# Performance work log

Hardware: AMD Instinct MI355X
Metric: run time of the kernel (lower is better)

Reference implementation:

```python
import jax, jax.numpy as jnp
import numpy as np

N = 4096   # in_features
M = 4096   # out_features
RANK, FT_RANK = 128, 64
Q_SCALE, R_SCALE, L_SCALE, GLOBAL_SCALE = 0.9, 1.05, 1.1, 1.0


def fwht(x):
    """Normalized fast Walsh-Hadamard transform over last dim (power of 2).
    Matches matmul_hadU/hadUt for power-of-2 sizes (H symmetric, 1/sqrt(n))."""
    B, n = x.shape
    y, h = x, 1
    while h < n:
        y = y.reshape(B, n // (2 * h), 2, h)
        a, b = y[:, :, 0, :], y[:, :, 1, :]
        y = jnp.stack((a + b, a - b), axis=2)
        h *= 2
    return y.reshape(B, n) * (1.0 / np.sqrt(n)).astype(np.float32)


def dequant(grid, idxs, scale, n_cols):
    # E8P dequant: gather 8-dim lattice vectors, reshape to [rows, n_cols].
    return grid[idxs].reshape(idxs.shape[0], n_cols) * jnp.float32(scale)


def setup_inputs() -> dict:
    key = jax.random.key(0)
    ks = jax.random.split(key, 9)
    return {
        "x": jax.random.normal(ks[0], (4, 2048, N), jnp.float32),
        "SU": jnp.sign(jax.random.normal(ks[1], (N,), jnp.float32)),
        "SV": jnp.sign(jax.random.normal(ks[2], (M,), jnp.float32)),
        "grid": jax.random.normal(ks[3], (65536, 8), jnp.float32) * 0.05,
        "L_ft": jax.random.normal(ks[4], (M, FT_RANK), jnp.float32) * 0.05,
        "R_ft": jax.random.normal(ks[5], (FT_RANK, N), jnp.float32) * 0.05,
        "Q_idxs": jax.random.randint(ks[6], (M, N // 8), 0, 65536, jnp.int32),
        "R_idxs": jax.random.randint(ks[7], (RANK - FT_RANK, N // 8), 0, 65536, jnp.int32),
        "L_idxs": jax.random.randint(ks[8], (RANK - FT_RANK, M // 8), 0, 65536, jnp.int32),
    }


def reference(x, SU, SV, grid, L_ft, R_ft, Q_idxs, R_idxs, L_idxs):
    shape = x.shape
    xf = x.reshape(-1, N) * SU            # [T, n]
    xh = fwht(xf)                          # left randomized Hadamard (hadUt)
    # Q path (x/32 then *scale*32 cancels; applied via scale on W).
    W_q = dequant(grid, Q_idxs, Q_SCALE, N)          # [m, n]
    out = xh @ W_q.T                                  # [T, m]
    # Quantized low-rank path: xR = x @ W_R^T; out += xR @ W_L (transposed L).
    W_r = dequant(grid, R_idxs, R_SCALE, N)           # [r, n]
    W_l = dequant(grid, L_idxs, L_SCALE, M)           # [r, m]
    xR = xh @ W_r.T                                   # [T, r]
    out = out + xR @ W_l                              # [T, m]
    # Fine-tunable LoRA path.
    out = out + (xh @ R_ft.T) @ L_ft.T                # [T, m]
    out = fwht(out)                                   # right Hadamard (hadU)
    out = out * SV * jnp.float32(GLOBAL_SCALE)
    return out.reshape(shape[:-1] + (M,))
```

## Files before the change

kernel.cpp:

```cpp
#include <hip/hip_runtime.h>
#include <stdint.h>
#include <stddef.h>


typedef __attribute__((ext_vector_type(8))) __bf16 bf16x8;
typedef __attribute__((ext_vector_type(4))) float f32x4;

#define DEVFN static __device__ __forceinline__

typedef const __attribute__((address_space(1))) void* as1cvp;
typedef __attribute__((address_space(3))) void* as3vp;

DEVFN void async_g2l16(const void* g, void* l) {
  __builtin_amdgcn_global_load_lds((as1cvp)g, (as3vp)l, 16, 0, 0);
}

DEVFN void fwht16(float* v) {
  #pragma unroll
  for (int h = 1; h < 16; h <<= 1) {
    #pragma unroll
    for (int i = 0; i < 16; ++i) {
      if ((i & h) == 0) {
        float a = v[i], b = v[i + h];
        v[i] = a + b;
        v[i + h] = a - b;
      }
    }
  }
}

DEVFN int padi(int i) { return i + (i >> 4) + (i >> 8); }

template<int MODE>
__global__ __launch_bounds__(256)
void fwht_rows(const float* in, const float* __restrict__ sgn,
               __bf16* __restrict__ outb, float* outf)
{
  __shared__ float s[4366];
  const int row = blockIdx.x;
  const int t = threadIdx.x;
  const int base1 = t * 17 + (t >> 4);
  float v[16];

  {
    const float* src = in + (size_t)row * 4096 + t * 16;
    #pragma unroll
    for (int j4 = 0; j4 < 4; ++j4) {
      f32x4 xv = *(const f32x4*)(src + j4 * 4);
      #pragma unroll
      for (int q = 0; q < 4; ++q) v[j4 * 4 + q] = xv[q];
    }
  }
  if (MODE == 0) {
    const f32x4* sg4 = (const f32x4*)(sgn + t * 16);
    #pragma unroll
    for (int j4 = 0; j4 < 4; ++j4) {
      f32x4 sv = sg4[j4];
      #pragma unroll
      for (int q = 0; q < 4; ++q) v[j4 * 4 + q] *= sv[q];
    }
  }
  fwht16(v);
  #pragma unroll
  for (int j = 0; j < 16; ++j) s[base1 + j] = v[j];
  __syncthreads();

  const int base2 = (t & 15) + ((t >> 4) << 8);
  #pragma unroll
  for (int i = 0; i < 16; ++i) v[i] = s[padi(base2 + (i << 4))];
  fwht16(v);
  #pragma unroll
  for (int i = 0; i < 16; ++i) s[padi(base2 + (i << 4))] = v[i];
  __syncthreads();

  #pragma unroll
  for (int i = 0; i < 16; ++i) v[i] = s[padi(t + (i << 8))];
  fwht16(v);
  #pragma unroll
  for (int i = 0; i < 16; ++i) s[padi(t + (i << 8))] = v[i];
  __syncthreads();

  if (MODE == 0) {
    bf16x8 o0, o1;
    #pragma unroll
    for (int j = 0; j < 8; ++j) o0[j] = (__bf16)(s[base1 + j] * 0.015625f);
    #pragma unroll
    for (int j = 0; j < 8; ++j) o1[j] = (__bf16)(s[base1 + 8 + j] * 0.015625f);
    __bf16* dst = outb + (size_t)row * 4096 + t * 16;
    *(bf16x8*)dst = o0;
    *(bf16x8*)(dst + 8) = o1;
  } else {
    const f32x4* sg4 = (const f32x4*)(sgn + t * 16);
    float* dst = outf + (size_t)row * 4096 + t * 16;
    #pragma unroll
    for (int j4 = 0; j4 < 4; ++j4) {
      f32x4 sv = sg4[j4];
      f32x4 ov;
      #pragma unroll
      for (int q = 0; q < 4; ++q) ov[q] = s[base1 + j4 * 4 + q] * 0.015625f * sv[q];
      *(f32x4*)(dst + j4 * 4) = ov;
    }
  }
}

__global__ __launch_bounds__(256)
void prep_uv(const float* __restrict__ grid8,
             const float* __restrict__ Lft, const float* __restrict__ Rft,
             const int* __restrict__ Lidx, const int* __restrict__ Ridx,
             __bf16* __restrict__ Ut, __bf16* __restrict__ Vt)
{
  int tid = blockIdx.x * 256 + threadIdx.x;
  const int half = 4096 * 128;
  bool isV = tid >= half;
  int e = isV ? tid - half : tid;
  int j = e >> 7;
  int r = e & 127;
  float v;
  if (!isV) {
    if (r < 64) v = 1.1f * grid8[(size_t)Lidx[r * 512 + (j >> 3)] * 8 + (j & 7)];
    else        v = Lft[(size_t)j * 64 + (r - 64)];
    Ut[e] = (__bf16)v;
  } else {
    if (r < 64) v = 1.05f * grid8[(size_t)Ridx[r * 512 + (j >> 3)] * 8 + (j & 7)];
    else        v = Rft[(size_t)(r - 64) * 4096 + j];
    Vt[e] = (__bf16)v;
  }
}

template<int K>
__global__ __launch_bounds__(256)
void gemm_bt(const __bf16* __restrict__ A, const __bf16* __restrict__ B,
             __bf16* __restrict__ Cb,
             const int* __restrict__ Qidx, const float* __restrict__ grid8,
             int Nn, int nbx)
{
  __shared__ __bf16 sA[128 * 64];
  __shared__ __bf16 sB[128 * 64];

  const int nwg = gridDim.x;
  const int orig = blockIdx.x;
  const int cpx = nwg >> 3;
  const int wg = (orig & 7) * cpx + (orig >> 3);
  const int bm = wg / nbx, bn = wg % nbx;

  const int t = threadIdx.x;
  const int lane = t & 63;
  const int w = t >> 6;
  const int wr = w >> 1, wc = w & 1;

  const int aRow0 = bm * 128;
  const int bRow0 = bn * 128;

  f32x4 acc[4][4] = {};

  #pragma unroll 1
  for (int k0 = 0; k0 < K; k0 += 64) {
    #pragma unroll
    for (int i = 0; i < 4; ++i) {
      int u = i * 256 + t;
      int rowu = u >> 3, cs = u & 7;
      int c = cs ^ (rowu & 7);
      async_g2l16(A + (size_t)(aRow0 + rowu) * K + k0 + c * 8, &sA[u * 8]);
      async_g2l16(B + (size_t)(bRow0 + rowu) * K + k0 + c * 8, &sB[u * 8]);
    }
    asm volatile("s_waitcnt vmcnt(0)" ::: "memory");
    __syncthreads();

    bf16x8 a[4][2], b[4][2];
    #pragma unroll
    for (int m = 0; m < 4; ++m) {
      #pragma unroll
      for (int kk = 0; kk < 2; ++kk) {
        int c = kk * 4 + (lane >> 4);
        int rowA = wr * 64 + m * 16 + (lane & 15);
        int uA = rowA * 8 + (c ^ (rowA & 7));
        a[m][kk] = *(const bf16x8*)&sA[uA * 8];
        int rowB = wc * 64 + m * 16 + (lane & 15);
        int uB = rowB * 8 + (c ^ (rowB & 7));
        b[m][kk] = *(const bf16x8*)&sB[uB * 8];
      }
    }
    #pragma unroll
    for (int kk = 0; kk < 2; ++kk)
      #pragma unroll
      for (int m = 0; m < 4; ++m)
        #pragma unroll
        for (int n = 0; n < 4; ++n)
          acc[m][n] = __builtin_amdgcn_mfma_f32_16x16x32_bf16(
              a[m][kk], b[n][kk], acc[m][n], 0, 0, 0);
    __syncthreads();
  }

  #pragma unroll
  for (int m = 0; m < 4; ++m) {
    #pragma unroll
    for (int n = 0; n < 4; ++n) {
      int gr = aRow0 + wr * 64 + m * 16 + ((lane >> 4) << 2);
      int gc = bRow0 + wc * 64 + n * 16 + (lane & 15);
      #pragma unroll
      for (int q = 0; q < 4; ++q) {
        float v = acc[m][n][q];
        int idx = Qidx[(size_t)(gr + q) * (Nn >> 3) + (gc >> 3)];
        v += 0.9f * grid8[(size_t)idx * 8 + (gc & 7)];
        Cb[(size_t)(gr + q) * Nn + gc] = (__bf16)v;
      }
    }
  }
}

template<int NT>
__global__ __launch_bounds__(512, 2)
void gemm256(const __bf16* __restrict__ A, const __bf16* __restrict__ B,
             float* __restrict__ Cf, int Nn, int nbx)
{
  constexpr int K = NT * 32;
  __shared__ __bf16 lds[4 * 2 * 8192];

  const int nwg = gridDim.x;
  const int orig = blockIdx.x;
  const int cpx = nwg >> 3;
  const int wg = (orig & 7) * cpx + (orig >> 3);
  const int bm = wg / nbx, bn = wg % nbx;

  const int tid = threadIdx.x;
  const int lane = tid & 63;
  const int wid = tid >> 6;
  const int wm = wid >> 2;
  const int wn = wid & 3;

  const int aRow0 = bm * 256;
  const int bRow0 = bn * 256;

  auto stage = [&](int t) {
    __bf16* dA = &lds[((t & 3) * 2 + 0) * 8192];
    __bf16* dB = &lds[((t & 3) * 2 + 1) * 8192];
    const __bf16* sAg = A + (size_t)aRow0 * K + t * 32;
    const __bf16* sBg = B + (size_t)bRow0 * K + t * 32;
    #pragma unroll
    for (int i = 0; i < 2; ++i) {
      int u = i * 512 + tid;
      int prow = u >> 3, slot = u & 7;
      int chunk = slot ^ (prow & 7);
      int r = 2 * prow + (chunk >> 2);
      int k8 = chunk & 3;
      async_g2l16(sAg + (size_t)r * K + k8 * 8, dA + u * 8);
    }
    #pragma unroll
    for (int i = 0; i < 2; ++i) {
      int u = i * 512 + tid;
      int prow = u >> 3, slot = u & 7;
      int chunk = slot ^ (prow & 7);
      int r = 2 * prow + (chunk >> 2);
      int k8 = chunk & 3;
      async_g2l16(sBg + (size_t)r * K + k8 * 8, dB + u * 8);
    }
  };

  const int k8l = lane >> 4;
  const int rl = lane & 15;

  f32x4 acc[8][4] = {};

  stage(0); stage(1); stage(2);
  asm volatile("s_waitcnt vmcnt(8)" ::: "memory");
  __syncthreads();

  #pragma unroll 1
  for (int t = 0; t < NT; ++t) {
    if (t + 3 < NT) stage(t + 3);

    const __bf16* bufA = &lds[((t & 3) * 2 + 0) * 8192];
    const __bf16* bufB = &lds[((t & 3) * 2 + 1) * 8192];

    bf16x8 af[8], bfr[4];
    #pragma unroll
    for (int m = 0; m < 8; ++m) {
      int r = wm * 128 + m * 16 + rl;
      int prow = r >> 1;
      int slot = (((r & 1) << 2) | k8l) ^ (prow & 7);
      af[m] = *(const bf16x8*)(bufA + (prow * 8 + slot) * 8);
    }
    #pragma unroll
    for (int n = 0; n < 4; ++n) {
      int r = wn * 64 + n * 16 + rl;
      int prow = r >> 1;
      int slot = (((r & 1) << 2) | k8l) ^ (prow & 7);
      bfr[n] = *(const bf16x8*)(bufB + (prow * 8 + slot) * 8);
    }

    __builtin_amdgcn_s_setprio(1);
    #pragma unroll
    for (int m = 0; m < 8; ++m)
      #pragma unroll
      for (int n = 0; n < 4; ++n)
        acc[m][n] = __builtin_amdgcn_mfma_f32_16x16x32_bf16(
            af[m], bfr[n], acc[m][n], 0, 0, 0);
    __builtin_amdgcn_s_setprio(0);

    if (t + 3 < NT)      asm volatile("s_waitcnt vmcnt(8)" ::: "memory");
    else if (t + 2 < NT) asm volatile("s_waitcnt vmcnt(4)" ::: "memory");
    else if (t + 1 < NT) asm volatile("s_waitcnt vmcnt(0)" ::: "memory");
    __syncthreads();
  }

  #pragma unroll
  for (int m = 0; m < 8; ++m) {
    #pragma unroll
    for (int n = 0; n < 4; ++n) {
      int gr = aRow0 + wm * 128 + m * 16 + ((lane >> 4) << 2);
      int gc = bRow0 + wn * 64 + n * 16 + (lane & 15);
      #pragma unroll
      for (int q = 0; q < 4; ++q)
        Cf[(size_t)(gr + q) * Nn + gc] = acc[m][n][q];
    }
  }
}

extern "C" void kernel_launch(void* const* d_in, const int* in_sizes, int n_in,
                              void* d_out, int out_size, void* d_ws, size_t ws_size,
                              hipStream_t stream) {
  const float* x    = (const float*)d_in[0];
  const float* SU   = (const float*)d_in[1];
  const float* SV   = (const float*)d_in[2];
  const float* grid = (const float*)d_in[3];
  const float* Lft  = (const float*)d_in[4];
  const float* Rft  = (const float*)d_in[5];
  const int*   Qidx = (const int*)d_in[6];
  const int*   Ridx = (const int*)d_in[7];
  const int*   Lidx = (const int*)d_in[8];
  float* out = (float*)d_out;

  char* ws = (char*)d_ws;
  __bf16* xh = (__bf16*)ws;
  __bf16* Wc = (__bf16*)(ws + ((size_t)64 << 20));
  __bf16* Ut = (__bf16*)(ws + ((size_t)96 << 20));
  __bf16* Vt = (__bf16*)(ws + ((size_t)97 << 20));

  prep_uv<<<4096, 256, 0, stream>>>(grid, Lft, Rft, Lidx, Ridx, Ut, Vt);
  fwht_rows<0><<<8192, 256, 0, stream>>>(x, SU, xh, nullptr);
  gemm_bt<128><<<1024, 256, 0, stream>>>(Ut, Vt, Wc, Qidx, grid, 4096, 32);
  gemm256<128><<<512, 512, 0, stream>>>(xh, Wc, out, 4096, 16);
  fwht_rows<1><<<8192, 256, 0, stream>>>(out, SV, nullptr, out);
}
```

Measured before the change: 589.6 us.

## Restructure main GEMM into 8-phase ping-pong pipeline and batch FWHT rows per block

The main bf16 GEMM now uses K-tiles of 64 with double buffering instead of K=32 with a 4-stage ring. Each iteration is split into four MFMA quadrants, with LDS fragment loads and the next tile's global-to-LDS copies interleaved between explicit barriers, to overlap memory traffic with matrix-core work. The FWHT row kernel now handles 4 rows per block, loading signs once and prefetching the next row while the current one finishes. It also writes the last butterfly stage directly from registers with strided stores, dropping one LDS round trip. Risks are extra barriers, register pressure from the larger fragment arrays, and less coalesced output stores in the FWHT kernel.

```diff
diff --git a/kernel.cpp b/kernel.cpp
--- a/kernel.cpp
+++ b/kernel.cpp
@@ -34,72 +34,82 @@
 template<int MODE>
 __global__ __launch_bounds__(256)
 void fwht_rows(const float* in, const float* __restrict__ sgn,
-               __bf16* __restrict__ outb, float* outf)
+               __bf16* __restrict__ outb, float* __restrict__ outf)
 {
   __shared__ float s[4366];
-  const int row = blockIdx.x;
   const int t = threadIdx.x;
   const int base1 = t * 17 + (t >> 4);
-  float v[16];
-
+  const int base2 = (t & 15) + ((t >> 4) << 8);
+
+  float sg[16];
+  if (MODE == 0) {
+    const f32x4* p = (const f32x4*)(sgn + t * 16);
+    #pragma unroll
+    for (int j4 = 0; j4 < 4; ++j4) {
+      f32x4 sv = p[j4];
+      #pragma unroll
+      for (int q = 0; q < 4; ++q) sg[j4 * 4 + q] = sv[q];
+    }
+  } else {
+    #pragma unroll
+    for (int i = 0; i < 16; ++i) sg[i] = sgn[t + (i << 8)];
+  }
+
+  float v[16], w[16];
+  const int row0 = blockIdx.x * 4;
   {
-    const float* src = in + (size_t)row * 4096 + t * 16;
+    const f32x4* p = (const f32x4*)(in + (size_t)row0 * 4096 + t * 16);
     #pragma unroll
     for (int j4 = 0; j4 < 4; ++j4) {
-      f32x4 xv = *(const f32x4*)(src + j4 * 4);
+      f32x4 xv = p[j4];
       #pragma unroll
       for (int q = 0; q < 4; ++q) v[j4 * 4 + q] = xv[q];
     }
   }
-  if (MODE == 0) {
-    const f32x4* sg4 = (const f32x4*)(sgn + t * 16);
-    #pragma unroll
-    for (int j4 = 0; j4 < 4; ++j4) {
-      f32x4 sv = sg4[j4];
-      #pragma unroll
-      for (int q = 0; q < 4; ++q) v[j4 * 4 + q] *= sv[q];
-    }
-  }
-  fwht16(v);
-  #pragma unroll
-  for (int j = 0; j < 16; ++j) s[base1 + j] = v[j];
-  __syncthreads();
-
-  const int base2 = (t & 15) + ((t >> 4) << 8);
-  #pragma unroll
-  for (int i = 0; i < 16; ++i) v[i] = s[padi(base2 + (i << 4))];
-  fwht16(v);
-  #pragma unroll
-  for (int i = 0; i < 16; ++i) s[padi(base2 + (i << 4))] = v[i];
-  __syncthreads();
-
-  #pragma unroll
-  for (int i = 0; i < 16; ++i) v[i] = s[padi(t + (i << 8))];
-  fwht16(v);
-  #pragma unroll
-  for (int i = 0; i < 16; ++i) s[padi(t + (i << 8))] = v[i];
-  __syncthreads();
-
-  if (MODE == 0) {
-    bf16x8 o0, o1;
-    #pragma unroll
-    for (int j = 0; j < 8; ++j) o0[j] = (__bf16)(s[base1 + j] * 0.015625f);
-    #pragma unroll
-    for (int j = 0; j < 8; ++j) o1[j] = (__bf16)(s[base1 + 8 + j] * 0.015625f);
-    __bf16* dst = outb + (size_t)row * 4096 + t * 16;
-    *(bf16x8*)dst = o0;
-    *(bf16x8*)(dst + 8) = o1;
-  } else {
-    const f32x4* sg4 = (const f32x4*)(sgn + t * 16);
-    float* dst = outf + (size_t)row * 4096 + t * 16;
-    #pragma unroll
-    for (int j4 = 0; j4 < 4; ++j4) {
-      f32x4 sv = sg4[j4];
-      f32x4 ov;
-      #pragma unroll
-      for (int q = 0; q < 4; ++q) ov[q] = s[base1 + j4 * 4 + q] * 0.015625f * sv[q];
-      *(f32x4*)(dst + j4 * 4) = ov;
-    }
+
+  #pragma unroll 1
+  for (int rr = 0; rr < 4; ++rr) {
+    const int row = row0 + rr;
+    if (MODE == 0) {
+      #pragma unroll
+      for (int i = 0; i < 16; ++i) v[i] *= sg[i];
+    }
+    fwht16(v);
+    #pragma unroll
+    for (int j = 0; j < 16; ++j) s[base1 + j] = v[j];
+    __syncthreads();
+
+    #pragma unroll
+    for (int i = 0; i < 16; ++i) v[i] = s[padi(base2 + (i << 4))];
+    fwht16(v);
+    #pragma unroll
+    for (int i = 0; i < 16; ++i) s[padi(base2 + (i << 4))] = v[i];
+    __syncthreads();
+
+    #pragma unroll
+    for (int i = 0; i < 16; ++i) w[i] = s[padi(t + (i << 8))];
+
+    if (rr < 3) {
+      const f32x4* p = (const f32x4*)(in + (size_t)(row + 1) * 4096 + t * 16);
+      #pragma unroll
+      for (int j4 = 0; j4 < 4; ++j4) {
+        f32x4 xv = p[j4];
+        #pragma unroll
+        for (int q = 0; q < 4; ++q) v[j4 * 4 + q] = xv[q];
+      }
+    }
+
+    fwht16(w);
+    if (MODE == 0) {
+      #pragma unroll
+      for (int i = 0; i < 16; ++i)
+        outb[(size_t)row * 4096 + t + (i << 8)] = (__bf16)(w[i] * 0.015625f);
+    } else {
+      #pragma unroll
+      for (int i = 0; i < 16; ++i)
+        outf[(size_t)row * 4096 + t + (i << 8)] = w[i] * 0.015625f * sg[i];
+    }
+    __syncthreads();
   }
 }
 
@@ -210,11 +220,11 @@
 
 template<int NT>
 __global__ __launch_bounds__(512, 2)
-void gemm256(const __bf16* __restrict__ A, const __bf16* __restrict__ B,
-             float* __restrict__ Cf, int Nn, int nbx)
+void gemm256_8p(const __bf16* __restrict__ A, const __bf16* __restrict__ B,
+                float* __restrict__ Cf, int Nn, int nbx)
 {
-  constexpr int K = NT * 32;
-  __shared__ __bf16 lds[4 * 2 * 8192];
+  constexpr int K = NT * 64;
+  __shared__ __bf16 lds[2 * 32768];
 
   const int nwg = gridDim.x;
   const int orig = blockIdx.x;
@@ -231,76 +241,143 @@
   const int aRow0 = bm * 256;
   const int bRow0 = bn * 256;
 
-  auto stage = [&](int t) {
-    __bf16* dA = &lds[((t & 3) * 2 + 0) * 8192];
-    __bf16* dB = &lds[((t & 3) * 2 + 1) * 8192];
-    const __bf16* sAg = A + (size_t)aRow0 * K + t * 32;
-    const __bf16* sBg = B + (size_t)bRow0 * K + t * 32;
-    #pragma unroll
-    for (int i = 0; i < 2; ++i) {
-      int u = i * 512 + tid;
-      int prow = u >> 3, slot = u & 7;
-      int chunk = slot ^ (prow & 7);
-      int r = 2 * prow + (chunk >> 2);
-      int k8 = chunk & 3;
-      async_g2l16(sAg + (size_t)r * K + k8 * 8, dA + u * 8);
-    }
-    #pragma unroll
-    for (int i = 0; i < 2; ++i) {
-      int u = i * 512 + tid;
-      int prow = u >> 3, slot = u & 7;
-      int chunk = slot ^ (prow & 7);
-      int r = 2 * prow + (chunk >> 2);
-      int k8 = chunk & 3;
-      async_g2l16(sBg + (size_t)r * K + k8 * 8, dB + u * 8);
-    }
-  };
-
   const int k8l = lane >> 4;
   const int rl = lane & 15;
 
+  auto stageA = [&](int t) {
+    __bf16* d = &lds[(t & 1) * 32768];
+    const __bf16* g = A + (size_t)aRow0 * K + t * 64;
+    #pragma unroll
+    for (int i = 0; i < 4; ++i) {
+      int u = i * 512 + tid;
+      int row = u >> 3, slot = u & 7;
+      int chunk = slot ^ (row & 7);
+      async_g2l16(g + (size_t)row * K + chunk * 8, d + u * 8);
+    }
+  };
+  auto stageB = [&](int t) {
+    __bf16* d = &lds[(t & 1) * 32768 + 16384];
+    const __bf16* g = B + (size_t)bRow0 * K + t * 64;
+    #pragma unroll
+    for (int i = 0; i < 4; ++i) {
+      int u = i * 512 + tid;
+      int row = u >> 3, slot = u & 7;
+      int chunk = slot ^ (row & 7);
+      async_g2l16(g + (size_t)row * K + chunk * 8, d + u * 8);
+    }
+  };
+
   f32x4 acc[8][4] = {};
 
-  stage(0); stage(1); stage(2);
+  stageA(0); stageB(0); stageA(1); stageB(1);
   asm volatile("s_waitcnt vmcnt(8)" ::: "memory");
-  __syncthreads();
+  __builtin_amdgcn_sched_barrier(0);
+  __builtin_amdgcn_s_barrier();
+  __builtin_amdgcn_sched_barrier(0);
+
+  bf16x8 a[8][2], b[4][2];
 
   #pragma unroll 1
   for (int t = 0; t < NT; ++t) {
-    if (t + 3 < NT) stage(t + 3);
-
-    const __bf16* bufA = &lds[((t & 3) * 2 + 0) * 8192];
-    const __bf16* bufB = &lds[((t & 3) * 2 + 1) * 8192];
-
-    bf16x8 af[8], bfr[4];
-    #pragma unroll
-    for (int m = 0; m < 8; ++m) {
-      int r = wm * 128 + m * 16 + rl;
-      int prow = r >> 1;
-      int slot = (((r & 1) << 2) | k8l) ^ (prow & 7);
-      af[m] = *(const bf16x8*)(bufA + (prow * 8 + slot) * 8);
-    }
-    #pragma unroll
-    for (int n = 0; n < 4; ++n) {
-      int r = wn * 64 + n * 16 + rl;
-      int prow = r >> 1;
-      int slot = (((r & 1) << 2) | k8l) ^ (prow & 7);
-      bfr[n] = *(const bf16x8*)(bufB + (prow * 8 + slot) * 8);
-    }
-
+    const __bf16* bufA = &lds[(t & 1) * 32768];
+    const __bf16* bufB = &lds[(t & 1) * 32768 + 16384];
+
+    #pragma unroll
+    for (int m = 0; m < 4; ++m)
+      #pragma unroll
+      for (int kk = 0; kk < 2; ++kk) {
+        int row = wm * 128 + m * 16 + rl;
+        int slot = (kk * 4 + k8l) ^ (row & 7);
+        a[m][kk] = *(const bf16x8*)(bufA + (row * 8 + slot) * 8);
+      }
+    #pragma unroll
+    for (int n = 0; n < 2; ++n)
+      #pragma unroll
+      for (int kk = 0; kk < 2; ++kk) {
+        int row = wn * 64 + n * 16 + rl;
+        int slot = (kk * 4 + k8l) ^ (row & 7);
+        b[n][kk] = *(const bf16x8*)(bufB + (row * 8 + slot) * 8);
+      }
+    __builtin_amdgcn_s_barrier();
+    asm volatile("s_waitcnt lgkmcnt(0)" ::: "memory");
+    __builtin_amdgcn_sched_barrier(0);
     __builtin_amdgcn_s_setprio(1);
     #pragma unroll
-    for (int m = 0; m < 8; ++m)
-      #pragma unroll
-      for (int n = 0; n < 4; ++n)
-        acc[m][n] = __builtin_amdgcn_mfma_f32_16x16x32_bf16(
-            af[m], bfr[n], acc[m][n], 0, 0, 0);
+    for (int kk = 0; kk < 2; ++kk)
+      #pragma unroll
+      for (int m = 0; m < 4; ++m)
+        #pragma unroll
+        for (int n = 0; n < 2; ++n)
+          acc[m][n] = __builtin_amdgcn_mfma_f32_16x16x32_bf16(
+              a[m][kk], b[n][kk], acc[m][n], 0, 0, 0);
     __builtin_amdgcn_s_setprio(0);
-
-    if (t + 3 < NT)      asm volatile("s_waitcnt vmcnt(8)" ::: "memory");
-    else if (t + 2 < NT) asm volatile("s_waitcnt vmcnt(4)" ::: "memory");
+    __builtin_amdgcn_s_barrier();
+
+    #pragma unroll
+    for (int m = 4; m < 8; ++m)
+      #pragma unroll
+      for (int kk = 0; kk < 2; ++kk) {
+        int row = wm * 128 + m * 16 + rl;
+        int slot = (kk * 4 + k8l) ^ (row & 7);
+        a[m][kk] = *(const bf16x8*)(bufA + (row * 8 + slot) * 8);
+      }
+    #pragma unroll
+    for (int n = 2; n < 4; ++n)
+      #pragma unroll
+      for (int kk = 0; kk < 2; ++kk) {
+        int row = wn * 64 + n * 16 + rl;
+        int slot = (kk * 4 + k8l) ^ (row & 7);
+        b[n][kk] = *(const bf16x8*)(bufB + (row * 8 + slot) * 8);
+      }
+    __builtin_amdgcn_s_barrier();
+    asm volatile("s_waitcnt lgkmcnt(0)" ::: "memory");
+    __builtin_amdgcn_sched_barrier(0);
+    __builtin_amdgcn_s_setprio(1);
+    #pragma unroll
+    for (int kk = 0; kk < 2; ++kk)
+      #pragma unroll
+      for (int m = 0; m < 4; ++m)
+        #pragma unroll
+        for (int n = 2; n < 4; ++n)
+          acc[m][n] = __builtin_amdgcn_mfma_f32_16x16x32_bf16(
+              a[m][kk], b[n][kk], acc[m][n], 0, 0, 0);
+    __builtin_amdgcn_s_setprio(0);
+    __builtin_amdgcn_s_barrier();
+
+    __builtin_amdgcn_sched_barrier(0);
+    if (t + 2 < NT) stageA(t + 2);
+    __builtin_amdgcn_s_barrier();
+    __builtin_amdgcn_s_setprio(1);
+    #pragma unroll
+    for (int kk = 0; kk < 2; ++kk)
+      #pragma unroll
+      for (int m = 4; m < 8; ++m)
+        #pragma unroll
+        for (int n = 0; n < 2; ++n)
+          acc[m][n] = __builtin_amdgcn_mfma_f32_16x16x32_bf16(
+              a[m][kk], b[n][kk], acc[m][n], 0, 0, 0);
+    __builtin_amdgcn_s_setprio(0);
+    __builtin_amdgcn_s_barrier();
+
+    __builtin_amdgcn_sched_barrier(0);
+    if (t + 2 < NT) stageB(t + 2);
+    __builtin_amdgcn_s_barrier();
+    __builtin_amdgcn_s_setprio(1);
+    #pragma unroll
+    for (int kk = 0; kk < 2; ++kk)
+      #pragma unroll
+      for (int m = 4; m < 8; ++m)
+        #pragma unroll
+        for (int n = 2; n < 4; ++n)
+          acc[m][n] = __builtin_amdgcn_mfma_f32_16x16x32_bf16(
+              a[m][kk], b[n][kk], acc[m][n], 0, 0, 0);
+    __builtin_amdgcn_s_setprio(0);
+
+    if (t + 2 < NT)      asm volatile("s_waitcnt vmcnt(8)" ::: "memory");
     else if (t + 1 < NT) asm volatile("s_waitcnt vmcnt(0)" ::: "memory");
-    __syncthreads();
+    __builtin_amdgcn_sched_barrier(0);
+    __builtin_amdgcn_s_barrier();
+    __builtin_amdgcn_sched_barrier(0);
   }
 
   #pragma unroll
@@ -308,7 +385,7 @@
     #pragma unroll
     for (int n = 0; n < 4; ++n) {
       int gr = aRow0 + wm * 128 + m * 16 + ((lane >> 4) << 2);
-      int gc = bRow0 + wn * 64 + n * 16 + (lane & 15);
+      int gc = bRow0 + wn * 64 + n * 16 + rl;
       #pragma unroll
       for (int q = 0; q < 4; ++q)
         Cf[(size_t)(gr + q) * Nn + gc] = acc[m][n][q];
@@ -337,8 +414,8 @@
   __bf16* Vt = (__bf16*)(ws + ((size_t)97 << 20));
 
   prep_uv<<<4096, 256, 0, stream>>>(grid, Lft, Rft, Lidx, Ridx, Ut, Vt);
-  fwht_rows<0><<<8192, 256, 0, stream>>>(x, SU, xh, nullptr);
+  fwht_rows<0><<<2048, 256, 0, stream>>>(x, SU, xh, nullptr);
   gemm_bt<128><<<1024, 256, 0, stream>>>(Ut, Vt, Wc, Qidx, grid, 4096, 32);
-  gemm256<128><<<512, 512, 0, stream>>>(xh, Wc, out, 4096, 16);
-  fwht_rows<1><<<8192, 256, 0, stream>>>(out, SV, nullptr, out);
-}
+  gemm256_8p<64><<<512, 512, 0, stream>>>(xh, Wc, out, 4096, 16);
+  fwht_rows<1><<<2048, 256, 0, stream>>>(out, SV, nullptr, out);
+}
```

New measurement: 572.0 us. 1.03x faster.
